# Kernel tuning notes

Hardware: AMD Instinct MI355X
Metric: run time of the kernel (lower is better)

## Reference

```python
import jax, jax.numpy as jnp
import numpy as np

B, Himg, Wimg, C, NH = 16, 64, 64, 256, 8
HD = C // NH  # 32
N = Himg * Wimg  # 4096


def _rotations(h, w, hd):
    # RMT/RAVLT 2D axial RoPE: head_dim split into two halves (rows, cols),
    # each half holds k_max = hd//4 complex frequencies.
    k_max = hd // 4
    theta = 1.0 / (10000.0 ** (np.arange(k_max) / k_max))
    ang_h = np.arange(h)[:, None] * theta  # (h, k_max)
    ang_w = np.arange(w)[:, None] * theta  # (w, k_max)
    ang = np.concatenate([
        np.broadcast_to(ang_h[:, None, :], (h, w, k_max)),
        np.broadcast_to(ang_w[None, :, :], (h, w, k_max)),
    ], axis=-1)  # (h, w, hd//2)
    return jnp.asarray(np.cos(ang), jnp.float32), jnp.asarray(np.sin(ang), jnp.float32)

COS, SIN = _rotations(Himg, Wimg, HD)


def _rope(x):
    # x: (b, nh, H, W, hd); complex rotation of (even, odd) channel pairs
    xr, xi = x[..., 0::2], x[..., 1::2]
    out_r = xr * COS - xi * SIN
    out_i = xr * SIN + xi * COS
    return jnp.stack([out_r, out_i], axis=-1).reshape(x.shape)


def setup_inputs() -> dict:
    key = jax.random.key(0)
    ks = jax.random.split(key, 5)
    return {
        "x": jax.random.normal(ks[0], (B, N, C), jnp.float32),
        "w_qkvo": jax.random.normal(ks[1], (C, 4 * C), jnp.float32) * 0.02,
        "b_qkvo": jnp.zeros((4 * C,), jnp.float32),
        "lepe_w": jax.random.normal(ks[2], (C, 1, 5, 5), jnp.float32) * 0.02,
        "lepe_b": jnp.zeros((C,), jnp.float32),
        "w_proj": jax.random.normal(ks[3], (C, C), jnp.float32) * 0.02,
        "b_proj": jnp.zeros((C,), jnp.float32),
    }


def reference(x, w_qkvo, b_qkvo, lepe_w, lepe_b, w_proj, b_proj):
    b, n, c = x.shape
    scale = HD ** -0.5
    qkvo = x @ w_qkvo + b_qkvo  # (b, n, 4c)
    q, k, v, o = (qkvo[..., i * c:(i + 1) * c] for i in range(4))
    # LePE: depthwise 5x5 conv on v viewed as an image
    v_img = v.reshape(b, Himg, Wimg, c).transpose(0, 3, 1, 2)  # NCHW
    lepe = jax.lax.conv_general_dilated(
        v_img, lepe_w, window_strides=(1, 1), padding=[(2, 2), (2, 2)],
        dimension_numbers=("NCHW", "OIHW", "NCHW"), feature_group_count=c,
    ) + lepe_b[None, :, None, None]
    # ELU+1 feature map
    q = jax.nn.elu(q) + 1.0
    k = jax.nn.elu(k) + 1.0
    q = q.reshape(b, n, NH, HD).transpose(0, 2, 1, 3)  # (b, nh, n, hd)
    k = k.reshape(b, n, NH, HD).transpose(0, 2, 1, 3)
    v = v.reshape(b, n, NH, HD).transpose(0, 2, 1, 3)
    # efficiency reweighting of keys
    q_mean = q.mean(axis=-2, keepdims=True)  # (b, nh, 1, hd)
    eff = jax.nn.softmax(scale * jnp.einsum("bhod,bhnd->bhon", q_mean, k), axis=-1)
    k = k * eff.transpose(0, 1, 3, 2) * n  # (b, nh, n, hd)
    # RoPE on q and reweighted k
    q_rope = _rope(q.reshape(b, NH, Himg, Wimg, HD)).reshape(b, NH, n, HD)
    k_rope = _rope(k.reshape(b, NH, Himg, Wimg, HD)).reshape(b, NH, n, HD)
    # normalizer from non-rope q and mean of reweighted k
    z = 1.0 / (jnp.einsum("bhnd,bhod->bhno", q, k.mean(axis=-2, keepdims=True)) + 1e-6)
    # linear attention: kv accumulation then q @ kv (scale n^-1 split as n^-0.5 each)
    inv_sqrt_n = n ** -0.5
    kv = jnp.einsum("bhnd,bhne->bhde", k_rope * inv_sqrt_n, v * inv_sqrt_n)  # (b, nh, hd, hd)
    out = jnp.einsum("bhnd,bhde->bhne", q_rope, kv) * z
    out = out.transpose(0, 2, 1, 3).reshape(b, n, c)
    out = out + lepe.transpose(0, 2, 3, 1).reshape(b, n, c)
    out = out * o  # gate
    return out @ w_proj + b_proj
```

## Files before the change

### kernel.cpp

```cpp
#include <hip/hip_runtime.h>
#include <math.h>

constexpr int B   = 16;
constexpr int IH  = 64;
constexpr int IW  = 64;
constexpr int C   = 256;
constexpr int NH  = 8;
constexpr int HD  = 32;
constexpr int N   = IH * IW;
constexpr int C4  = 4 * C;
constexpr int KVP_STRIDE = 1060;

using f16x8 = __attribute__((ext_vector_type(8))) _Float16;
using f32x4 = __attribute__((ext_vector_type(4))) float;

__global__ void k_prologue(const float* __restrict__ w_qkvo,
                           const float* __restrict__ w_proj,
                           float* __restrict__ cosT, float* __restrict__ sinT,
                           _Float16* __restrict__ wqh, _Float16* __restrict__ wql,
                           _Float16* __restrict__ wph, _Float16* __restrict__ wpl) {
  int bid = blockIdx.x;
  int tid = threadIdx.x;
  if (bid < 256) {
    int t = bid * 256 + tid;
    int j = t & 15, pix = t >> 4;
    int y = pix >> 6, x = pix & 63;
    int jj = j & 7;
    double theta = pow(10000.0, -(double)jj / 8.0);
    double pos = (j < 8) ? (double)y : (double)x;
    double ang = pos * theta;
    cosT[t] = (float)cos(ang);
    sinT[t] = (float)sin(ang);
  } else if (bid < 256 + C4) {
    int n = bid - 256;
    float v = w_qkvo[(size_t)tid * C4 + n];
    _Float16 h = (_Float16)v;
    wqh[(size_t)n * 256 + tid] = h;
    wql[(size_t)n * 256 + tid] = (_Float16)(v - (float)h);
  } else {
    int n = bid - 256 - C4;
    float v = w_proj[(size_t)tid * C + n];
    _Float16 h = (_Float16)v;
    wph[(size_t)n * 256 + tid] = h;
    wpl[(size_t)n * 256 + tid] = (_Float16)(v - (float)h);
  }
}

__global__ __launch_bounds__(256) void k_gemm_split(
    const float* __restrict__ A, int lda,
    const _Float16* __restrict__ BhT, const _Float16* __restrict__ BlT,
    const float* __restrict__ bias, float* __restrict__ Cm, int ldc,
    int nelu, float* __restrict__ qpart) {
  __shared__ _Float16 lds[4 * 5120];
  _Float16* AhL = lds;
  _Float16* AlL = lds + 5120;
  _Float16* BhL = lds + 10240;
  _Float16* BlL = lds + 15360;
  int t = threadIdx.x;
  int m0 = blockIdx.x * 128, n0 = blockIdx.y * 128;
  int lane = t & 63;
  int wm = t >> 7, wn = (t >> 6) & 1;
  int lr = lane & 15, lg = lane >> 4;
  int srow = t >> 1, sseg = t & 1;

  f32x4 acc[4][4] = {};

  const float* aP = &A[(size_t)(m0 + srow) * lda + sseg * 16];
  const _Float16* bhP = &BhT[(size_t)(n0 + srow) * 256 + sseg * 16];
  const _Float16* blP = &BlT[(size_t)(n0 + srow) * 256 + sseg * 16];
  float4 ar0 = *(const float4*)(aP + 0);
  float4 ar1 = *(const float4*)(aP + 4);
  float4 ar2 = *(const float4*)(aP + 8);
  float4 ar3 = *(const float4*)(aP + 12);
  f16x8 brh0 = *(const f16x8*)(bhP + 0);
  f16x8 brh1 = *(const f16x8*)(bhP + 8);
  f16x8 brl0 = *(const f16x8*)(blP + 0);
  f16x8 brl1 = *(const f16x8*)(blP + 8);

  for (int kc = 0; kc < 256; kc += 32) {
    {
      float av[16] = {ar0.x, ar0.y, ar0.z, ar0.w, ar1.x, ar1.y, ar1.z, ar1.w,
                      ar2.x, ar2.y, ar2.z, ar2.w, ar3.x, ar3.y, ar3.z, ar3.w};
      f16x8 h0, h1, l0, l1;
#pragma unroll
      for (int j = 0; j < 8; ++j) {
        _Float16 h = (_Float16)av[j];
        h0[j] = h; l0[j] = (_Float16)(av[j] - (float)h);
        _Float16 h2 = (_Float16)av[j + 8];
        h1[j] = h2; l1[j] = (_Float16)(av[j + 8] - (float)h2);
      }
      int d = srow * 40 + sseg * 16;
      *(f16x8*)&AhL[d] = h0; *(f16x8*)&AhL[d + 8] = h1;
      *(f16x8*)&AlL[d] = l0; *(f16x8*)&AlL[d + 8] = l1;
      *(f16x8*)&BhL[d] = brh0; *(f16x8*)&BhL[d + 8] = brh1;
      *(f16x8*)&BlL[d] = brl0; *(f16x8*)&BlL[d + 8] = brl1;
    }
    __syncthreads();

    if (kc + 32 < 256) {
      const float* aN = aP + kc + 32;
      const _Float16* bhN = bhP + kc + 32;
      const _Float16* blN = blP + kc + 32;
      ar0 = *(const float4*)(aN + 0);
      ar1 = *(const float4*)(aN + 4);
      ar2 = *(const float4*)(aN + 8);
      ar3 = *(const float4*)(aN + 12);
      brh0 = *(const f16x8*)(bhN + 0);
      brh1 = *(const f16x8*)(bhN + 8);
      brl0 = *(const f16x8*)(blN + 0);
      brl1 = *(const f16x8*)(blN + 8);
    }

    f16x8 ah[4], al[4];
#pragma unroll
    for (int mi = 0; mi < 4; ++mi) {
      int ar = (wm * 64 + mi * 16 + lr) * 40 + lg * 8;
      ah[mi] = *(const f16x8*)&AhL[ar];
      al[mi] = *(const f16x8*)&AlL[ar];
    }
#pragma unroll
    for (int ni = 0; ni < 4; ++ni) {
      int br = (wn * 64 + ni * 16 + lr) * 40 + lg * 8;
      f16x8 bh = *(const f16x8*)&BhL[br];
      f16x8 bl = *(const f16x8*)&BlL[br];
#pragma unroll
      for (int mi = 0; mi < 4; ++mi) {
        acc[mi][ni] = __builtin_amdgcn_mfma_f32_16x16x32_f16(ah[mi], bh, acc[mi][ni], 0, 0, 0);
        acc[mi][ni] = __builtin_amdgcn_mfma_f32_16x16x32_f16(al[mi], bh, acc[mi][ni], 0, 0, 0);
        acc[mi][ni] = __builtin_amdgcn_mfma_f32_16x16x32_f16(ah[mi], bl, acc[mi][ni], 0, 0, 0);
      }
    }
    __syncthreads();
  }

  float* Cl = reinterpret_cast<float*>(lds);
  int ri2 = t >> 3, c0 = (t & 7) << 4;
  bool doq = (qpart != nullptr) && (n0 < 256);
  float qs[16] = {};
#pragma unroll
  for (int mi = 0; mi < 4; ++mi) {
#pragma unroll
    for (int ni = 0; ni < 4; ++ni) {
      int col = wn * 64 + ni * 16 + lr;
#pragma unroll
      for (int r = 0; r < 4; ++r)
        Cl[(wm * 16 + lg * 4 + r) * 132 + col] = acc[mi][ni][r];
    }
    __syncthreads();
    int grow = m0 + (ri2 >> 4) * 64 + mi * 16 + (ri2 & 15);
#pragma unroll
    for (int j = 0; j < 4; ++j) {
      int col = n0 + c0 + j * 4;
      float4 v = *(const float4*)&Cl[ri2 * 132 + c0 + j * 4];
      float4 bb = *(const float4*)&bias[col];
      v.x += bb.x; v.y += bb.y; v.z += bb.z; v.w += bb.w;
      if (col < nelu) {
        v.x = (v.x > 0.f) ? v.x + 1.f : expf(v.x);
        v.y = (v.y > 0.f) ? v.y + 1.f : expf(v.y);
        v.z = (v.z > 0.f) ? v.z + 1.f : expf(v.z);
        v.w = (v.w > 0.f) ? v.w + 1.f : expf(v.w);
      }
      if (doq) {
        qs[j * 4 + 0] += v.x; qs[j * 4 + 1] += v.y;
        qs[j * 4 + 2] += v.z; qs[j * 4 + 3] += v.w;
      }
      *(float4*)&Cm[(size_t)grow * ldc + col] = v;
    }
    __syncthreads();
  }
  if (doq) {
#pragma unroll
    for (int j = 0; j < 4; ++j) {
      float4 w4 = {qs[j*4+0], qs[j*4+1], qs[j*4+2], qs[j*4+3]};
      *(float4*)&Cl[ri2 * 132 + c0 + j * 4] = w4;
    }
    __syncthreads();
    if (t < 128) {
      float ssum = 0.f;
#pragma unroll
      for (int rr = 0; rr < 32; ++rr) ssum += Cl[rr * 132 + t];
      int b_local = m0 >> 12, rowblk = (m0 >> 7) & 31;
      qpart[(size_t)(b_local * 32 + rowblk) * 256 + n0 + t] = ssum;
    }
  }
}

__global__ __launch_bounds__(256) void k_kvflash_lepe(
    const float* __restrict__ qkvo, const float* __restrict__ qpart,
    const float* __restrict__ cosT, const float* __restrict__ sinT,
    float* __restrict__ kvp,
    const float* __restrict__ lepe_w, const float* __restrict__ lepe_b,
    float* __restrict__ lepe_out, int b0, int kvN) {
  __shared__ float qm[32];
  __shared__ float sL[512];
  __shared__ float red[256];
  __shared__ float ktG[4][32][36];
  __shared__ float vtG[4][32][36];
  int bid = blockIdx.x;
  int t = threadIdx.x;

  if (bid >= kvN) {
    int blk = bid - kvN;
    int b = blk >> 8, rem = blk & 255;
    int y = rem >> 2, x0 = (rem & 3) << 4;
    int c = t;
    float w[25];
#pragma unroll
    for (int i = 0; i < 25; ++i) w[i] = lepe_w[c * 25 + i];
    float bias = lepe_b[c];
    float acc[16];
#pragma unroll
    for (int p = 0; p < 16; ++p) acc[p] = bias;
#pragma unroll
    for (int dy = 0; dy < 5; ++dy) {
      int yy = y + dy - 2;
      if (yy < 0 || yy >= IH) continue;
      size_t rowb = (size_t)(b * N + (yy << 6)) * C4 + 512 + c;
#pragma unroll
      for (int dx = 0; dx < 5; ++dx) {
        float wv = w[dy * 5 + dx];
#pragma unroll
        for (int p = 0; p < 16; ++p) {
          int xx = x0 + p + dx - 2;
          if (xx < 0 || xx >= IW) continue;
          acc[p] = fmaf(qkvo[rowb + (size_t)xx * C4], wv, acc[p]);
        }
      }
    }
#pragma unroll
    for (int p = 0; p < 16; ++p)
      lepe_out[(size_t)((b0 + b) * N + (y << 6) + x0 + p) * C + c] = acc[p];
    return;
  }

  int bh = bid >> 3, chunk = bid & 7;
  int b = bh >> 3, h = bh & 7;
  int nbase = chunk << 9;

  if (t < 32) {
    float s = 0.f;
#pragma unroll
    for (int rb = 0; rb < 32; ++rb)
      s += qpart[(size_t)(b * 32 + rb) * 256 + (h << 5) + t];
    qm[t] = s * (1.0f / N) * 0.1767766952966369f;
  }
  __syncthreads();

  float qmr[32];
#pragma unroll
  for (int i = 0; i < 32; ++i) qmr[i] = qm[i];
  float mx = -3.4e38f;
#pragma unroll
  for (int i = 0; i < 2; ++i) {
    int n = nbase + t + i * 256;
    const float* kp = &qkvo[(size_t)(b * N + n) * C4 + 256 + (h << 5)];
    float dot = 0.f;
#pragma unroll
    for (int j = 0; j < 8; ++j) {
      float4 k4 = *(const float4*)(kp + (j << 2));
      dot += k4.x * qmr[j*4] + k4.y * qmr[j*4+1] + k4.z * qmr[j*4+2] + k4.w * qmr[j*4+3];
    }
    sL[t + i * 256] = dot;
    mx = fmaxf(mx, dot);
  }
  red[t] = mx; __syncthreads();
  for (int off = 128; off > 0; off >>= 1) {
    if (t < off) red[t] = fmaxf(red[t], red[t + off]);
    __syncthreads();
  }
  float mx_c = red[0];
  __syncthreads();
  float psum = expf(sL[t] - mx_c) + expf(sL[t + 256] - mx_c);
  red[t] = psum; __syncthreads();
  for (int off = 128; off > 0; off >>= 1) {
    if (t < off) red[t] += red[t + off];
    __syncthreads();
  }
  float sum_c = red[0];

  int sg = t >> 6;
  int lane = t & 63;
  int d0 = (lane >> 3) << 2;
  int e0 = (lane & 7) << 2;
  int srow_l = (t >> 1) & 31;
  int sdh = t & 1;
  float acc[4][4] = {};
  float km16[16] = {};

  for (int s = 0; s < 4; ++s) {
    int nloc = sg * 128 + s * 32 + srow_l;
    int n = nbase + nloc;
    const float* kp = &qkvo[(size_t)(b * N + n) * C4 + 256 + (h << 5) + sdh * 16];
    const float* vp = kp + 256;
    float ef = expf(sL[nloc] - mx_c);
    float kl[16], vl[16];
#pragma unroll
    for (int j4 = 0; j4 < 4; ++j4) {
      float4 k4 = *(const float4*)(kp + (j4 << 2));
      float4 v4 = *(const float4*)(vp + (j4 << 2));
      k4.x *= ef; k4.y *= ef; k4.z *= ef; k4.w *= ef;
      km16[j4*4+0] += k4.x; km16[j4*4+1] += k4.y;
      km16[j4*4+2] += k4.z; km16[j4*4+3] += k4.w;
      kl[j4*4+0] = k4.x; kl[j4*4+1] = k4.y; kl[j4*4+2] = k4.z; kl[j4*4+3] = k4.w;
      vl[j4*4+0] = v4.x; vl[j4*4+1] = v4.y; vl[j4*4+2] = v4.z; vl[j4*4+3] = v4.w;
    }
#pragma unroll
    for (int p = 0; p < 8; ++p) {
      float cc = cosT[(n << 4) + sdh * 8 + p];
      float sn = sinT[(n << 4) + sdh * 8 + p];
      float kr = kl[2*p], ki = kl[2*p+1];
      kl[2*p]   = kr * cc - ki * sn;
      kl[2*p+1] = kr * sn + ki * cc;
    }
#pragma unroll
    for (int j4 = 0; j4 < 4; ++j4) {
      float4 kw = {kl[j4*4+0], kl[j4*4+1], kl[j4*4+2], kl[j4*4+3]};
      float4 vw = {vl[j4*4+0], vl[j4*4+1], vl[j4*4+2], vl[j4*4+3]};
      *(float4*)&ktG[sg][srow_l][sdh*16 + (j4 << 2)] = kw;
      *(float4*)&vtG[sg][srow_l][sdh*16 + (j4 << 2)] = vw;
    }
    __syncthreads();
    __builtin_amdgcn_s_setprio(1);
#pragma unroll
    for (int nn = 0; nn < 32; ++nn) {
      float4 k4 = *(const float4*)&ktG[sg][nn][d0];
      float4 v4 = *(const float4*)&vtG[sg][nn][e0];
      float kv_[4] = {k4.x, k4.y, k4.z, k4.w};
      float vv_[4] = {v4.x, v4.y, v4.z, v4.w};
#pragma unroll
      for (int i = 0; i < 4; ++i)
#pragma unroll
        for (int j = 0; j < 4; ++j)
          acc[i][j] = fmaf(kv_[i], vv_[j], acc[i][j]);
    }
    __builtin_amdgcn_s_setprio(0);
    __syncthreads();
  }

  float* mrg = &ktG[0][0][0];
#pragma unroll
  for (int i = 0; i < 4; ++i)
#pragma unroll
    for (int j = 0; j < 4; ++j)
      mrg[sg * 1024 + (d0 + i) * 32 + (e0 + j)] = acc[i][j];
  __syncthreads();
  size_t o = (size_t)(bh * 8 + chunk) * KVP_STRIDE;
  {
    int idx = t << 2;
    float4 r;
    r.x = mrg[idx+0] + mrg[1024+idx+0] + mrg[2048+idx+0] + mrg[3072+idx+0];
    r.y = mrg[idx+1] + mrg[1024+idx+1] + mrg[2048+idx+1] + mrg[3072+idx+1];
    r.z = mrg[idx+2] + mrg[1024+idx+2] + mrg[2048+idx+2] + mrg[3072+idx+2];
    r.w = mrg[idx+3] + mrg[1024+idx+3] + mrg[2048+idx+3] + mrg[3072+idx+3];
    kvp[o + idx + 0] = r.x; kvp[o + idx + 1] = r.y;
    kvp[o + idx + 2] = r.z; kvp[o + idx + 3] = r.w;
  }
  float* kmb = &vtG[0][0][0];
#pragma unroll
  for (int j = 0; j < 16; ++j) kmb[t * 16 + j] = km16[j];
  __syncthreads();
  if (t < 32) {
    int dh = t >> 4, dj = t & 15;
    float ssum = 0.f;
    for (int r = 0; r < 128; ++r) ssum += kmb[((r << 1) + dh) * 16 + dj];
    kvp[o + 1024 + t] = ssum;
  }
  if (t == 0) {
    kvp[o + 1056] = mx_c;
    kvp[o + 1057] = sum_c;
  }
}

__global__ __launch_bounds__(256) void k_out_combine(
    float* __restrict__ qkvo, const float* __restrict__ kvp,
    const float* __restrict__ cosT, const float* __restrict__ sinT,
    const float* __restrict__ lepe, int b0) {
  __shared__ float kvs[1024];
  __shared__ float kms[32];
  __shared__ float fcs[8];
  int bh = blockIdx.x, chunk = blockIdx.y;
  int b = bh >> 3, h = bh & 7;
  int t = threadIdx.x;
  if (t == 0) {
    float mxs[8], sums[8];
    float mx = -3.4e38f;
#pragma unroll
    for (int c = 0; c < 8; ++c) {
      size_t o = (size_t)(bh * 8 + c) * KVP_STRIDE;
      mxs[c] = kvp[o + 1056];
      sums[c] = kvp[o + 1057];
      mx = fmaxf(mx, mxs[c]);
    }
    float T = 0.f;
#pragma unroll
    for (int c = 0; c < 8; ++c) T += sums[c] * expf(mxs[c] - mx);
    float invT = 1.0f / T;
#pragma unroll
    for (int c = 0; c < 8; ++c) fcs[c] = expf(mxs[c] - mx) * invT;
  }
  __syncthreads();
  {
    int idx = t << 2;
    size_t o0 = (size_t)(bh * 8) * KVP_STRIDE + idx;
    float4 r = {0.f, 0.f, 0.f, 0.f};
#pragma unroll
    for (int c = 0; c < 8; ++c) {
      float4 p = *(const float4*)&kvp[o0 + (size_t)c * KVP_STRIDE];
      float f = fcs[c];
      r.x += p.x * f; r.y += p.y * f; r.z += p.z * f; r.w += p.w * f;
    }
    *(float4*)&kvs[idx] = r;
    if (t < 32) {
      float s = 0.f;
#pragma unroll
      for (int c = 0; c < 8; ++c)
        s += kvp[(size_t)(bh * 8 + c) * KVP_STRIDE + 1024 + t] * fcs[c];
      kms[t] = s;
    }
  }
  __syncthreads();
  int n1 = (chunk << 8) + t;
  int n2 = n1 + 2048;
  size_t rb1 = (size_t)(b * N + n1) * C4;
  size_t rb2 = (size_t)(b * N + n2) * C4;
  float q1[32], q2[32];
#pragma unroll
  for (int i = 0; i < 8; ++i) {
    float4 a4 = *(const float4*)&qkvo[rb1 + (h << 5) + (i << 2)];
    float4 b4 = *(const float4*)&qkvo[rb2 + (h << 5) + (i << 2)];
    q1[i*4+0] = a4.x; q1[i*4+1] = a4.y; q1[i*4+2] = a4.z; q1[i*4+3] = a4.w;
    q2[i*4+0] = b4.x; q2[i*4+1] = b4.y; q2[i*4+2] = b4.z; q2[i*4+3] = b4.w;
  }
  float dot1 = 0.f, dot2 = 0.f;
#pragma unroll
  for (int dd = 0; dd < 32; ++dd) {
    dot1 += q1[dd] * kms[dd];
    dot2 += q2[dd] * kms[dd];
  }
  float zv1 = 1.0f / (dot1 + 1e-6f);
  float zv2 = 1.0f / (dot2 + 1e-6f);
#pragma unroll
  for (int j = 0; j < 16; ++j) {
    float c1 = cosT[(n1 << 4) + j], s1 = sinT[(n1 << 4) + j];
    float qr = q1[2*j], qi = q1[2*j+1];
    q1[2*j]   = qr * c1 - qi * s1;
    q1[2*j+1] = qr * s1 + qi * c1;
    float c2 = cosT[(n2 << 4) + j], s2 = sinT[(n2 << 4) + j];
    float kr = q2[2*j], ki = q2[2*j+1];
    q2[2*j]   = kr * c2 - ki * s2;
    q2[2*j+1] = kr * s2 + ki * c2;
  }
  size_t oc1 = (size_t)((b0 + b) * N + n1) * C + (h << 5);
  size_t oc2 = (size_t)((b0 + b) * N + n2) * C + (h << 5);
#pragma unroll
  for (int e4 = 0; e4 < 8; ++e4) {
    float a1x = 0, a1y = 0, a1z = 0, a1w = 0;
    float a2x = 0, a2y = 0, a2z = 0, a2w = 0;
#pragma unroll
    for (int dd = 0; dd < 32; ++dd) {
      float4 kv4 = *(const float4*)&kvs[(dd << 5) + (e4 << 2)];
      float qa = q1[dd], qb = q2[dd];
      a1x = fmaf(qa, kv4.x, a1x); a1y = fmaf(qa, kv4.y, a1y);
      a1z = fmaf(qa, kv4.z, a1z); a1w = fmaf(qa, kv4.w, a1w);
      a2x = fmaf(qb, kv4.x, a2x); a2y = fmaf(qb, kv4.y, a2y);
      a2z = fmaf(qb, kv4.z, a2z); a2w = fmaf(qb, kv4.w, a2w);
    }
    float4 lp1 = *(const float4*)&lepe[oc1 + (e4 << 2)];
    float4 ov1 = *(const float4*)&qkvo[rb1 + 768 + (h << 5) + (e4 << 2)];
    float4 r1;
    r1.x = (a1x * zv1 + lp1.x) * ov1.x;
    r1.y = (a1y * zv1 + lp1.y) * ov1.y;
    r1.z = (a1z * zv1 + lp1.z) * ov1.z;
    r1.w = (a1w * zv1 + lp1.w) * ov1.w;
    *(float4*)&qkvo[rb1 + (h << 5) + (e4 << 2)] = r1;
    float4 lp2 = *(const float4*)&lepe[oc2 + (e4 << 2)];
    float4 ov2 = *(const float4*)&qkvo[rb2 + 768 + (h << 5) + (e4 << 2)];
    float4 r2;
    r2.x = (a2x * zv2 + lp2.x) * ov2.x;
    r2.y = (a2y * zv2 + lp2.y) * ov2.y;
    r2.z = (a2z * zv2 + lp2.z) * ov2.z;
    r2.w = (a2w * zv2 + lp2.w) * ov2.w;
    *(float4*)&qkvo[rb2 + (h << 5) + (e4 << 2)] = r2;
  }
}

static inline size_t ws_bytes_needed(int bpp) {
  size_t pn = (size_t)bpp * N;
  size_t f32c = pn * C4
              + (size_t)bpp * 32 * 256
              + (size_t)bpp * NH * 8 * KVP_STRIDE
              + (size_t)N * 16 * 2;
  size_t f16c = (size_t)C * C4 * 2
              + (size_t)C * C * 2;
  return f32c * 4 + f16c * 2;
}

extern "C" void kernel_launch(void* const* d_in, const int* in_sizes, int n_in,
                              void* d_out, int out_size, void* d_ws, size_t ws_size,
                              hipStream_t stream) {
  const float* x      = (const float*)d_in[0];
  const float* w_qkvo = (const float*)d_in[1];
  const float* b_qkvo = (const float*)d_in[2];
  const float* lepe_w = (const float*)d_in[3];
  const float* lepe_b = (const float*)d_in[4];
  const float* w_proj = (const float*)d_in[5];
  const float* b_proj = (const float*)d_in[6];
  float* out = (float*)d_out;
  float* ws  = (float*)d_ws;

  int bpp = 2;
  if (ws_bytes_needed(16) <= ws_size) bpp = 16;
  else if (ws_bytes_needed(8) <= ws_size) bpp = 8;
  else if (ws_bytes_needed(4) <= ws_size) bpp = 4;

  size_t pn = (size_t)bpp * N;
  int nbh = bpp * NH;
  float* qkvo  = ws;
  float* qpart = qkvo  + pn * C4;
  float* kvp   = qpart + (size_t)bpp * 32 * 256;
  float* cosT  = kvp   + (size_t)nbh * 8 * KVP_STRIDE;
  float* sinT  = cosT  + (size_t)N * 16;
  _Float16* wqh = (_Float16*)(sinT + (size_t)N * 16);
  _Float16* wql = wqh + (size_t)C * C4;
  _Float16* wph = wql + (size_t)C * C4;
  _Float16* wpl = wph + (size_t)C * C;

  k_prologue<<<256 + C4 + C, 256, 0, stream>>>(w_qkvo, w_proj, cosT, sinT,
                                               wqh, wql, wph, wpl);

  for (int b0 = 0; b0 < B; b0 += bpp) {
    k_gemm_split<<<dim3(pn / 128, C4 / 128), 256, 0, stream>>>(
        x + (size_t)b0 * N * C, C, wqh, wql, b_qkvo, qkvo, C4, 512, qpart);
    int kvN = nbh * 8;
    k_kvflash_lepe<<<kvN + bpp * 256, 256, 0, stream>>>(
        qkvo, qpart, cosT, sinT, kvp, lepe_w, lepe_b, out, b0, kvN);
    k_out_combine<<<dim3(nbh, 8), 256, 0, stream>>>(qkvo, kvp, cosT, sinT, out, b0);
    k_gemm_split<<<dim3(pn / 128, C / 128), 256, 0, stream>>>(
        qkvo, C4, wph, wpl, b_proj, out + (size_t)b0 * N * C, C, 0, nullptr);
  }
}
```

Measured before the change: 441.5 us.

## Pre-pack split-fp16 weights in MFMA fragment order and load B directly from global

The prologue now writes the hi/lo fp16 weight copies in a packed layout that matches the MFMA 16x16x32 B-fragment lane order. The GEMM then has each wave load its B fragments straight from global memory (cached in L2) instead of staging them through LDS, which halves LDS use and removes the LDS writes and reads for B. The cost is that global loads now sit inside the compute loop with no software prefetch, so latency may be exposed, and each of the two M-waves fetches the same B data redundantly.

```diff
diff --git a/kernel.cpp b/kernel.cpp
--- a/kernel.cpp
+++ b/kernel.cpp
@@ -33,29 +33,33 @@
     sinT[t] = (float)sin(ang);
   } else if (bid < 256 + C4) {
     int n = bid - 256;
-    float v = w_qkvo[(size_t)tid * C4 + n];
+    int k = tid;
+    float v = w_qkvo[(size_t)k * C4 + n];
     _Float16 h = (_Float16)v;
-    wqh[(size_t)n * 256 + tid] = h;
-    wql[(size_t)n * 256 + tid] = (_Float16)(v - (float)h);
+    size_t idx = ((size_t)((n >> 4) * 8 + (k >> 5)) * 64 +
+                  (((k >> 3) & 3) * 16 + (n & 15))) * 8 + (k & 7);
+    wqh[idx] = h;
+    wql[idx] = (_Float16)(v - (float)h);
   } else {
     int n = bid - 256 - C4;
-    float v = w_proj[(size_t)tid * C + n];
+    int k = tid;
+    float v = w_proj[(size_t)k * C + n];
     _Float16 h = (_Float16)v;
-    wph[(size_t)n * 256 + tid] = h;
-    wpl[(size_t)n * 256 + tid] = (_Float16)(v - (float)h);
+    size_t idx = ((size_t)((n >> 4) * 8 + (k >> 5)) * 64 +
+                  (((k >> 3) & 3) * 16 + (n & 15))) * 8 + (k & 7);
+    wph[idx] = h;
+    wpl[idx] = (_Float16)(v - (float)h);
   }
 }
 
 __global__ __launch_bounds__(256) void k_gemm_split(
     const float* __restrict__ A, int lda,
-    const _Float16* __restrict__ BhT, const _Float16* __restrict__ BlT,
+    const _Float16* __restrict__ BhP, const _Float16* __restrict__ BlP,
     const float* __restrict__ bias, float* __restrict__ Cm, int ldc,
     int nelu, float* __restrict__ qpart) {
-  __shared__ _Float16 lds[4 * 5120];
+  __shared__ _Float16 lds[2 * 5120];
   _Float16* AhL = lds;
   _Float16* AlL = lds + 5120;
-  _Float16* BhL = lds + 10240;
-  _Float16* BlL = lds + 15360;
   int t = threadIdx.x;
   int m0 = blockIdx.x * 128, n0 = blockIdx.y * 128;
   int lane = t & 63;
@@ -66,16 +70,14 @@
   f32x4 acc[4][4] = {};
 
   const float* aP = &A[(size_t)(m0 + srow) * lda + sseg * 16];
-  const _Float16* bhP = &BhT[(size_t)(n0 + srow) * 256 + sseg * 16];
-  const _Float16* blP = &BlT[(size_t)(n0 + srow) * 256 + sseg * 16];
   float4 ar0 = *(const float4*)(aP + 0);
   float4 ar1 = *(const float4*)(aP + 4);
   float4 ar2 = *(const float4*)(aP + 8);
   float4 ar3 = *(const float4*)(aP + 12);
-  f16x8 brh0 = *(const f16x8*)(bhP + 0);
-  f16x8 brh1 = *(const f16x8*)(bhP + 8);
-  f16x8 brl0 = *(const f16x8*)(blP + 0);
-  f16x8 brl1 = *(const f16x8*)(blP + 8);
+
+  const int n16b = (n0 >> 4) + wn * 4;
+  const _Float16* bhW = BhP + (size_t)lane * 8;
+  const _Float16* blW = BlP + (size_t)lane * 8;
 
   for (int kc = 0; kc < 256; kc += 32) {
     {
@@ -92,25 +94,25 @@
       int d = srow * 40 + sseg * 16;
       *(f16x8*)&AhL[d] = h0; *(f16x8*)&AhL[d + 8] = h1;
       *(f16x8*)&AlL[d] = l0; *(f16x8*)&AlL[d + 8] = l1;
-      *(f16x8*)&BhL[d] = brh0; *(f16x8*)&BhL[d + 8] = brh1;
-      *(f16x8*)&BlL[d] = brl0; *(f16x8*)&BlL[d + 8] = brl1;
     }
     __syncthreads();
 
     if (kc + 32 < 256) {
       const float* aN = aP + kc + 32;
-      const _Float16* bhN = bhP + kc + 32;
-      const _Float16* blN = blP + kc + 32;
       ar0 = *(const float4*)(aN + 0);
       ar1 = *(const float4*)(aN + 4);
       ar2 = *(const float4*)(aN + 8);
       ar3 = *(const float4*)(aN + 12);
-      brh0 = *(const f16x8*)(bhN + 0);
-      brh1 = *(const f16x8*)(bhN + 8);
-      brl0 = *(const f16x8*)(blN + 0);
-      brl1 = *(const f16x8*)(blN + 8);
-    }
-
+    }
+
+    const int k32 = kc >> 5;
+    f16x8 bh[4], bl[4];
+#pragma unroll
+    for (int ni = 0; ni < 4; ++ni) {
+      size_t off = (size_t)((n16b + ni) * 8 + k32) * 512;
+      bh[ni] = *(const f16x8*)(bhW + off);
+      bl[ni] = *(const f16x8*)(blW + off);
+    }
     f16x8 ah[4], al[4];
 #pragma unroll
     for (int mi = 0; mi < 4; ++mi) {
@@ -120,14 +122,11 @@
     }
 #pragma unroll
     for (int ni = 0; ni < 4; ++ni) {
-      int br = (wn * 64 + ni * 16 + lr) * 40 + lg * 8;
-      f16x8 bh = *(const f16x8*)&BhL[br];
-      f16x8 bl = *(const f16x8*)&BlL[br];
 #pragma unroll
       for (int mi = 0; mi < 4; ++mi) {
-        acc[mi][ni] = __builtin_amdgcn_mfma_f32_16x16x32_f16(ah[mi], bh, acc[mi][ni], 0, 0, 0);
-        acc[mi][ni] = __builtin_amdgcn_mfma_f32_16x16x32_f16(al[mi], bh, acc[mi][ni], 0, 0, 0);
-        acc[mi][ni] = __builtin_amdgcn_mfma_f32_16x16x32_f16(ah[mi], bl, acc[mi][ni], 0, 0, 0);
+        acc[mi][ni] = __builtin_amdgcn_mfma_f32_16x16x32_f16(ah[mi], bh[ni], acc[mi][ni], 0, 0, 0);
+        acc[mi][ni] = __builtin_amdgcn_mfma_f32_16x16x32_f16(al[mi], bh[ni], acc[mi][ni], 0, 0, 0);
+        acc[mi][ni] = __builtin_amdgcn_mfma_f32_16x16x32_f16(ah[mi], bl[ni], acc[mi][ni], 0, 0, 0);
       }
     }
     __syncthreads();
```

Result: slower. 494.4 us (+12.0%).
